# Performance work log

Hardware: AMD Instinct MI355X
Metric: run time of the kernel (lower is better)

The kernel has to match this reference:

```python
import jax, jax.numpy as jnp
import numpy as np

C, N, B = 16, 65536, 4096  # cases, points per case, batch of case IDs


def _w(key, fan_in, fan_out):
    return jax.random.normal(key, (fan_in, fan_out), dtype=jnp.float32) / np.sqrt(fan_in).astype(np.float32)


def setup_inputs() -> dict:
    key = jax.random.key(0)
    ks = jax.random.split(key, 8)
    pts = jax.random.normal(ks[0], (C, N, 3), dtype=jnp.float32)
    inp = {
        "pts": pts,
        "W1_0": _w(ks[1], 3, 64), "b1_0": jnp.zeros((64,), jnp.float32),
        "W1_1": _w(ks[2], 64, 128), "b1_1": jnp.zeros((128,), jnp.float32),
        "W1_2": _w(ks[3], 128, 512), "b1_2": jnp.zeros((512,), jnp.float32),
        "W2_0": _w(ks[4], 512, 256), "b2_0": jnp.zeros((256,), jnp.float32),
        "W2_1": _w(ks[5], 256, 512), "b2_1": jnp.zeros((512,), jnp.float32),
        "x": jax.random.randint(ks[6], (B,), 0, C, dtype=jnp.int64),
    }
    return inp


def reference(pts, W1_0, b1_0, W1_1, b1_1, W1_2, b1_2, W2_0, b2_0, W2_1, b2_1, x):
    def mlp1(h):  # shared per-point MLP, SiLU after every layer
        h = jax.nn.silu(h @ W1_0 + b1_0)
        h = jax.nn.silu(h @ W1_1 + b1_1)
        h = jax.nn.silu(h @ W1_2 + b1_2)
        return h

    feats = mlp1(pts)                       # [C, N, F1]
    idx = jnp.argmax(feats, axis=1)         # [C, F1] critical-point indices per feature
    # gather critical points (detached in the torch original)
    fixed = jax.lax.stop_gradient(pts[jnp.arange(pts.shape[0])[:, None], idx])  # [C, F1, 3]

    feats2 = mlp1(fixed)                    # [C, F1, F1]
    latent0 = jnp.max(feats2, axis=1)       # [C, F1]

    h = jax.nn.silu(latent0 @ W2_0 + b2_0)  # [C, 256]
    latent = h @ W2_1 + b2_1                # [C, total_modes*ge_features]

    caseID_unit = jax.nn.one_hot(x, latent.shape[0], dtype=latent.dtype)  # [B, C]
    return caseID_unit @ latent             # [B, 512]
```

## Files before the change

### kernel.cpp

```cpp
#include <hip/hip_runtime.h>
#include <math.h>

#define NCASES   16
#define NPTS_BIG 65536
#define F1       512
#define OUT_B    4096

typedef __attribute__((ext_vector_type(8))) short  short8;
typedef __attribute__((ext_vector_type(4))) float  floatx4;

__device__ __forceinline__ float silu_f(float x) {
    return x * __builtin_amdgcn_rcpf(1.0f + __expf(-x));
}

__device__ __forceinline__ unsigned f2bf_hi(float x) {
    unsigned u = __float_as_uint(x);
    return u + 0x7FFFu + ((u >> 16) & 1u);
}
__device__ __forceinline__ unsigned short f2bf(float x) {
    return (unsigned short)(f2bf_hi(x) >> 16);
}
__device__ __forceinline__ unsigned pk2bf_rtz(float lo, float hi) {
    return __builtin_amdgcn_perm(__float_as_uint(hi), __float_as_uint(lo), 0x07060302u);
}

__device__ __forceinline__ unsigned enc_f(float x) {
    unsigned u = __float_as_uint(x);
    return (u & 0x80000000u) ? ~u : (u | 0x80000000u);
}
__device__ __forceinline__ float dec_f(unsigned e) {
    unsigned u = (e & 0x80000000u) ? (e ^ 0x80000000u) : ~e;
    return __uint_as_float(u);
}

__device__ __forceinline__ float sgpr_f(float x) {
    return __uint_as_float(__builtin_amdgcn_readfirstlane(__float_as_uint(x)));
}

__global__ void k_prep(const float* __restrict__ W11, const float* __restrict__ W12,
                       unsigned short* __restrict__ BbWs, unsigned short* __restrict__ BcWs,
                       unsigned long long* __restrict__ argBufs)
{
    int i = blockIdx.x * 256 + threadIdx.x;
    if (i < 16384) argBufs[i] = 0ull;
    {
        int j = i & 7, l = (i >> 3) & 63, t = i >> 9;
        int KT = t & 3, NT = (t >> 2) & 3, w = t >> 4;
        int k = KT * 32 + (l >> 4) * 8 + j;
        int f = w * 64 + NT * 16 + (l & 15);
        BcWs[i] = f2bf(W12[(size_t)k * 512 + f]);
    }
    if (i < 8192) {
        int j = i & 7, l = (i >> 3) & 63, t = i >> 9;
        int KT = t & 1, w = t >> 1;
        int k = KT * 32 + (l >> 4) * 8 + j;
        int f = w * 16 + (l & 15);
        BbWs[i] = f2bf(W11[(size_t)k * 128 + f]);
    }
}

template<bool GATHER>
__global__ __launch_bounds__(512, 4)
void k_mlp1_argmax(const float* __restrict__ pts, int nPts, int chunksPerBlock,
                   const unsigned long long* __restrict__ gatherIdx,
                   const float* __restrict__ W10, const float* __restrict__ b10,
                   const float* __restrict__ b11, const float* __restrict__ b12,
                   const unsigned short* __restrict__ BbWs,
                   const unsigned short* __restrict__ BcWs,
                   unsigned long long* __restrict__ argOut)
{
    const int c   = blockIdx.y;
    const int tid = threadIdx.x;
    const int w   = tid >> 6;
    const int l   = tid & 63;
    const int lm  = l & 15;
    const int q   = l >> 4;

    __shared__ __align__(16) unsigned short s_h0[2][64][72];
    __shared__ __align__(16) unsigned short s_h1[2][64][136];

    const int wf = __builtin_amdgcn_readfirstlane(w);

    float wA0[8], wA1[8], wA2[8], bA[8];
    #pragma unroll
    for (int j = 0; j < 8; ++j) {
        wA0[j] = sgpr_f(W10[  0 + wf * 8 + j]);
        wA1[j] = sgpr_f(W10[ 64 + wf * 8 + j]);
        wA2[j] = sgpr_f(W10[128 + wf * 8 + j]);
        bA[j]  = sgpr_f(b10[       wf * 8 + j]);
    }

    short8 Bc[16];
    #pragma unroll
    for (int t = 0; t < 16; ++t)
        Bc[t] = *(const short8*)(BcWs + (size_t)((wf * 16 + t) * 64 + l) * 8);
    short8 Bb[2];
    #pragma unroll
    for (int t = 0; t < 2; ++t)
        Bb[t] = *(const short8*)(BbWs + (size_t)((wf * 2 + t) * 64 + l) * 8);

    const float bias11 = b11[wf * 16 + lm];
    const floatx4 bias4 = {bias11, bias11, bias11, bias11};
    const floatx4 zero4 = {0.f, 0.f, 0.f, 0.f};

    const int colw = (wf * 16 + lm) ^ (q << 3);
    const int qx8  = ((q ^ ((lm >> 2) & 3)) << 3);

    float bestv[4];
    #pragma unroll
    for (int NT = 0; NT < 4; ++NT) bestv[NT] = -INFINITY;

    const float* cpts = pts + (size_t)c * nPts * 3;

    auto ldpt = [&](int ch, float& x, float& y, float& z) {
        const int pbase = (blockIdx.x * chunksPerBlock + ch) * 64;
        if (GATHER) {
            unsigned gi = ~(unsigned)(gatherIdx[(size_t)c * 512 + pbase + l] & 0xFFFFFFFFull);
            const float* sp = cpts + (size_t)gi * 3;
            x = sp[0]; y = sp[1]; z = sp[2];
        } else {
            const float* sp = cpts + (size_t)(pbase + l) * 3;
            x = sp[0]; y = sp[1]; z = sp[2];
        }
    };
    auto stageA = [&](int p, float x, float y, float z) {
        float v[8];
        #pragma unroll
        for (int j = 0; j < 8; ++j) {
            float t = fmaf(z, wA2[j], bA[j]);
            t = fmaf(y, wA1[j], t);
            t = fmaf(x, wA0[j], t);
            v[j] = silu_f(t);
        }
        uint4 hv = { pk2bf_rtz(v[0], v[1]), pk2bf_rtz(v[2], v[3]),
                     pk2bf_rtz(v[4], v[5]), pk2bf_rtz(v[6], v[7]) };
        *(uint4*)&s_h0[p][l][wf * 8] = hv;
    };

    {
        float x, y, z;
        ldpt(0, x, y, z);
        stageA(0, x, y, z);
    }
    __syncthreads();

    for (int ch = 0; ch < chunksPerBlock; ++ch) {
        const int p = ch & 1;
        const bool more = (ch + 1 < chunksPerBlock);

        float nx, ny, nz;
        if (more) ldpt(ch + 1, nx, ny, nz);

        #pragma unroll
        for (int MT = 0; MT < 4; ++MT) {
            short8 a0 = *(const short8*)&s_h0[p][MT * 16 + lm][q * 8];
            short8 a1 = *(const short8*)&s_h0[p][MT * 16 + lm][32 + q * 8];
            floatx4 acc = __builtin_amdgcn_mfma_f32_16x16x32_bf16(a0, Bb[0], bias4, 0, 0, 0);
            acc = __builtin_amdgcn_mfma_f32_16x16x32_bf16(a1, Bb[1], acc, 0, 0, 0);
            #pragma unroll
            for (int r = 0; r < 4; ++r) {
                unsigned uv = __float_as_uint(silu_f(acc[r]));
                s_h1[p][MT * 16 + q * 4 + r][colw] = (unsigned short)(uv >> 16);
            }
        }

        if (more) stageA(p ^ 1, nx, ny, nz);

        __syncthreads();

        const int cb0 = 127 - (ch << 4);
        #pragma unroll
        for (int MT = 0; MT < 4; ++MT) {
            short8 a[4];
            #pragma unroll
            for (int KT = 0; KT < 4; ++KT)
                a[KT] = *(const short8*)&s_h1[p][MT * 16 + lm][KT * 32 + qx8];
            const int cbM = cb0 - (MT << 2);
            #pragma unroll
            for (int NT = 0; NT < 4; ++NT) {
                floatx4 acc = __builtin_amdgcn_mfma_f32_16x16x32_bf16(a[0], Bc[NT * 4 + 0], zero4, 0, 0, 0);
                #pragma unroll
                for (int KT = 1; KT < 4; ++KT)
                    acc = __builtin_amdgcn_mfma_f32_16x16x32_bf16(a[KT], Bc[NT * 4 + KT], acc, 0, 0, 0);
                float x0 = __uint_as_float((__float_as_uint(acc[0]) & 0xFFFFFF80u) | (unsigned)(cbM));
                float x1 = __uint_as_float((__float_as_uint(acc[1]) & 0xFFFFFF80u) | (unsigned)(cbM - 1));
                float x2 = __uint_as_float((__float_as_uint(acc[2]) & 0xFFFFFF80u) | (unsigned)(cbM - 2));
                float x3 = __uint_as_float((__float_as_uint(acc[3]) & 0xFFFFFF80u) | (unsigned)(cbM - 3));
                float t0 = fmaxf(fmaxf(x0, x1), x2);
                bestv[NT] = fmaxf(fmaxf(t0, x3), bestv[NT]);
            }
        }
    }

    #pragma unroll
    for (int NT = 0; NT < 4; ++NT) {
        unsigned u = __float_as_uint(bestv[NT]);
        int t = 127 - (int)(u & 127u);
        unsigned idx = (unsigned)((blockIdx.x * chunksPerBlock + (t >> 4)) * 64
                                  + ((t >> 2) & 3) * 16 + q * 4 + (t & 3));
        float v = __uint_as_float(u & 0xFFFFFF80u) + b12[wf * 64 + NT * 16 + lm];
        #pragma unroll
        for (int m = 16; m <= 32; m <<= 1) {
            float    vo = __shfl_xor(v, m, 64);
            unsigned io = __shfl_xor(idx, m, 64);
            if (vo > v || (vo == v && io < idx)) { v = vo; idx = io; }
        }
        if (q == 0) {
            unsigned long long key = ((unsigned long long)enc_f(v) << 32)
                                   | (unsigned long long)(~idx);
            atomicMax(&argOut[(size_t)c * 512 + wf * 64 + NT * 16 + lm], key);
        }
    }
}

__global__ __launch_bounds__(256)
void k_head(const unsigned long long* __restrict__ argBuf2,
            const float* __restrict__ W20, const float* __restrict__ b20,
            const float* __restrict__ W21, const float* __restrict__ b21,
            float* __restrict__ latent)
{
    const int c = blockIdx.x, tid = threadIdx.x;
    __shared__ float l0[512];
    __shared__ float hh[256];
    l0[tid]       = silu_f(dec_f((unsigned)(argBuf2[(size_t)c * 512 + tid] >> 32)));
    l0[tid + 256] = silu_f(dec_f((unsigned)(argBuf2[(size_t)c * 512 + tid + 256] >> 32)));
    __syncthreads();
    float acc = b20[tid];
    for (int k = 0; k < 512; ++k) acc += l0[k] * W20[(size_t)k * 256 + tid];
    hh[tid] = silu_f(acc);
    __syncthreads();
    #pragma unroll
    for (int r = 0; r < 2; ++r) {
        int f = tid + r * 256;
        float a2 = b21[f];
        for (int k = 0; k < 256; ++k) a2 += hh[k] * W21[(size_t)k * 512 + f];
        latent[(size_t)c * 512 + f] = a2;
    }
}

__global__ void k_scatter(const int* __restrict__ x,
                          const float* __restrict__ latent,
                          float* __restrict__ out)
{
    const int b = blockIdx.x, t = threadIdx.x;
    int cid = x[b];
    const float4* src = (const float4*)(latent + (size_t)cid * 512);
    float4* dst = (float4*)(out + (size_t)b * 512);
    dst[t] = src[t];
}

extern "C" void kernel_launch(void* const* d_in, const int* in_sizes, int n_in,
                              void* d_out, int out_size, void* d_ws, size_t ws_size,
                              hipStream_t stream)
{
    const float* pts = (const float*)d_in[0];
    const float* W10 = (const float*)d_in[1];
    const float* b10 = (const float*)d_in[2];
    const float* W11 = (const float*)d_in[3];
    const float* b11 = (const float*)d_in[4];
    const float* W12 = (const float*)d_in[5];
    const float* b12 = (const float*)d_in[6];
    const float* W20 = (const float*)d_in[7];
    const float* b20 = (const float*)d_in[8];
    const float* W21 = (const float*)d_in[9];
    const float* b21 = (const float*)d_in[10];
    const int*   x   = (const int*)d_in[11];
    float* out = (float*)d_out;

    char* ws = (char*)d_ws;
    unsigned long long* argBuf  = (unsigned long long*)ws;
    unsigned long long* argBuf2 = (unsigned long long*)(ws + 65536);
    float* latent               = (float*)(ws + 131072);
    unsigned short* BbWs        = (unsigned short*)(ws + 163840);
    unsigned short* BcWs        = (unsigned short*)(ws + 180224);

    k_prep<<<dim3(256), dim3(256), 0, stream>>>(W11, W12, BbWs, BcWs, argBuf);

    k_mlp1_argmax<false><<<dim3(128, NCASES), dim3(512), 0, stream>>>(
        pts, NPTS_BIG, 8, nullptr, W10, b10, b11, b12, BbWs, BcWs, argBuf);

    k_mlp1_argmax<true><<<dim3(8, NCASES), dim3(512), 0, stream>>>(
        pts, NPTS_BIG, 1, argBuf, W10, b10, b11, b12, BbWs, BcWs, argBuf2);

    k_head<<<dim3(NCASES), dim3(256), 0, stream>>>(argBuf2, W20, b20, W21, b21, latent);

    k_scatter<<<dim3(OUT_B), dim3(128), 0, stream>>>(x, latent, out);
}
```

Before: 264.9 us.

## Software-pipeline MLP stages across chunks with one barrier per chunk

Restructures the per-chunk loop into a three-stage software pipeline. Layer 3 (the argmax GEMM) for chunk ch now runs in the same barrier region as layer 2 for chunk ch+1 and layer 1 for chunk ch+2. Layer-2 MFMAs are interleaved per MT with layer-3 MFMAs, and the loop is unrolled by two so the buffer pointers stay static. The aim is to cut the number of barriers per chunk and overlap the small layer-2 work and the point loads with the big layer-3 MFMAs. The cost is a longer prologue and higher register pressure from interleaving.

```diff
diff --git a/kernel.cpp b/kernel.cpp
--- a/kernel.cpp
+++ b/kernel.cpp
@@ -8,6 +8,7 @@
 
 typedef __attribute__((ext_vector_type(8))) short  short8;
 typedef __attribute__((ext_vector_type(4))) float  floatx4;
+typedef unsigned short ush;
 
 __device__ __forceinline__ float silu_f(float x) {
     return x * __builtin_amdgcn_rcpf(1.0f + __expf(-x));
@@ -17,8 +18,8 @@
     unsigned u = __float_as_uint(x);
     return u + 0x7FFFu + ((u >> 16) & 1u);
 }
-__device__ __forceinline__ unsigned short f2bf(float x) {
-    return (unsigned short)(f2bf_hi(x) >> 16);
+__device__ __forceinline__ ush f2bf(float x) {
+    return (ush)(f2bf_hi(x) >> 16);
 }
 __device__ __forceinline__ unsigned pk2bf_rtz(float lo, float hi) {
     return __builtin_amdgcn_perm(__float_as_uint(hi), __float_as_uint(lo), 0x07060302u);
@@ -38,7 +39,7 @@
 }
 
 __global__ void k_prep(const float* __restrict__ W11, const float* __restrict__ W12,
-                       unsigned short* __restrict__ BbWs, unsigned short* __restrict__ BcWs,
+                       ush* __restrict__ BbWs, ush* __restrict__ BcWs,
                        unsigned long long* __restrict__ argBufs)
 {
     int i = blockIdx.x * 256 + threadIdx.x;
@@ -65,8 +66,8 @@
                    const unsigned long long* __restrict__ gatherIdx,
                    const float* __restrict__ W10, const float* __restrict__ b10,
                    const float* __restrict__ b11, const float* __restrict__ b12,
-                   const unsigned short* __restrict__ BbWs,
-                   const unsigned short* __restrict__ BcWs,
+                   const ush* __restrict__ BbWs,
+                   const ush* __restrict__ BcWs,
                    unsigned long long* __restrict__ argOut)
 {
     const int c   = blockIdx.y;
@@ -76,8 +77,8 @@
     const int lm  = l & 15;
     const int q   = l >> 4;
 
-    __shared__ __align__(16) unsigned short s_h0[2][64][72];
-    __shared__ __align__(16) unsigned short s_h1[2][64][136];
+    __shared__ __align__(16) ush s_h0[2][64][72];
+    __shared__ __align__(16) ush s_h1[2][64][136];
 
     const int wf = __builtin_amdgcn_readfirstlane(w);
 
@@ -123,7 +124,7 @@
             x = sp[0]; y = sp[1]; z = sp[2];
         }
     };
-    auto stageA = [&](int p, float x, float y, float z) {
+    auto stageA = [&](ush (*H0)[72], float x, float y, float z) {
         float v[8];
         #pragma unroll
         for (int j = 0; j < 8; ++j) {
@@ -134,47 +135,32 @@
         }
         uint4 hv = { pk2bf_rtz(v[0], v[1]), pk2bf_rtz(v[2], v[3]),
                      pk2bf_rtz(v[4], v[5]), pk2bf_rtz(v[6], v[7]) };
-        *(uint4*)&s_h0[p][l][wf * 8] = hv;
+        *(uint4*)&H0[l][wf * 8] = hv;
     };
-
-    {
-        float x, y, z;
-        ldpt(0, x, y, z);
-        stageA(0, x, y, z);
-    }
-    __syncthreads();
-
-    for (int ch = 0; ch < chunksPerBlock; ++ch) {
-        const int p = ch & 1;
-        const bool more = (ch + 1 < chunksPerBlock);
-
+    auto stageB_MT = [&](ush (*H0)[72], ush (*H1)[136], int MT) {
+        short8 a0 = *(const short8*)&H0[MT * 16 + lm][q * 8];
+        short8 a1 = *(const short8*)&H0[MT * 16 + lm][32 + q * 8];
+        floatx4 acc = __builtin_amdgcn_mfma_f32_16x16x32_bf16(a0, Bb[0], bias4, 0, 0, 0);
+        acc = __builtin_amdgcn_mfma_f32_16x16x32_bf16(a1, Bb[1], acc, 0, 0, 0);
+        #pragma unroll
+        for (int r = 0; r < 4; ++r) {
+            unsigned uv = __float_as_uint(silu_f(acc[r]));
+            H1[MT * 16 + q * 4 + r][colw] = (ush)(uv >> 16);
+        }
+    };
+
+    auto region = [&](int ch, ush (*H1C)[136], ush (*H1B)[136],
+                      ush (*H0B)[72], ush (*H0A)[72], bool haveB, bool haveA) {
         float nx, ny, nz;
-        if (more) ldpt(ch + 1, nx, ny, nz);
-
-        #pragma unroll
-        for (int MT = 0; MT < 4; ++MT) {
-            short8 a0 = *(const short8*)&s_h0[p][MT * 16 + lm][q * 8];
-            short8 a1 = *(const short8*)&s_h0[p][MT * 16 + lm][32 + q * 8];
-            floatx4 acc = __builtin_amdgcn_mfma_f32_16x16x32_bf16(a0, Bb[0], bias4, 0, 0, 0);
-            acc = __builtin_amdgcn_mfma_f32_16x16x32_bf16(a1, Bb[1], acc, 0, 0, 0);
-            #pragma unroll
-            for (int r = 0; r < 4; ++r) {
-                unsigned uv = __float_as_uint(silu_f(acc[r]));
-                s_h1[p][MT * 16 + q * 4 + r][colw] = (unsigned short)(uv >> 16);
-            }
-        }
-
-        if (more) stageA(p ^ 1, nx, ny, nz);
-
-        __syncthreads();
-
+        if (haveA) ldpt(ch + 2, nx, ny, nz);
         const int cb0 = 127 - (ch << 4);
         #pragma unroll
         for (int MT = 0; MT < 4; ++MT) {
             short8 a[4];
             #pragma unroll
             for (int KT = 0; KT < 4; ++KT)
-                a[KT] = *(const short8*)&s_h1[p][MT * 16 + lm][KT * 32 + qx8];
+                a[KT] = *(const short8*)&H1C[MT * 16 + lm][KT * 32 + qx8];
+            if (haveB) stageB_MT(H0B, H1B, MT);
             const int cbM = cb0 - (MT << 2);
             #pragma unroll
             for (int NT = 0; NT < 4; ++NT) {
@@ -190,6 +176,32 @@
                 bestv[NT] = fmaxf(fmaxf(t0, x3), bestv[NT]);
             }
         }
+        if (haveA) stageA(H0A, nx, ny, nz);
+        __syncthreads();
+    };
+
+    {
+        float x, y, z;
+        ldpt(0, x, y, z);
+        stageA(s_h0[0], x, y, z);
+    }
+    __syncthreads();
+    {
+        float x = 0.f, y = 0.f, z = 0.f;
+        const bool have1 = (chunksPerBlock > 1);
+        if (have1) ldpt(1, x, y, z);
+        #pragma unroll
+        for (int MT = 0; MT < 4; ++MT) stageB_MT(s_h0[0], s_h1[0], MT);
+        if (have1) stageA(s_h0[1], x, y, z);
+    }
+    __syncthreads();
+
+    for (int ch = 0; ch < chunksPerBlock; ch += 2) {
+        region(ch,     s_h1[0], s_h1[1], s_h0[1], s_h0[0],
+               ch + 1 < chunksPerBlock, ch + 2 < chunksPerBlock);
+        if (ch + 1 < chunksPerBlock)
+            region(ch + 1, s_h1[1], s_h1[0], s_h0[0], s_h0[1],
+                   ch + 2 < chunksPerBlock, ch + 3 < chunksPerBlock);
     }
 
     #pragma unroll
@@ -271,8 +283,8 @@
     unsigned long long* argBuf  = (unsigned long long*)ws;
     unsigned long long* argBuf2 = (unsigned long long*)(ws + 65536);
     float* latent               = (float*)(ws + 131072);
-    unsigned short* BbWs        = (unsigned short*)(ws + 163840);
-    unsigned short* BcWs        = (unsigned short*)(ws + 180224);
+    ush* BbWs                   = (ush*)(ws + 163840);
+    ush* BcWs                   = (ush*)(ws + 180224);
 
     k_prep<<<dim3(256), dim3(256), 0, stream>>>(W11, W12, BbWs, BcWs, argBuf);
 
```

Measured after the change: 856.7 us. +223.4%, slower.
